# Kernel tuning notes

Hardware: AMD Instinct MI355X
Metric: run time of the kernel (lower is better)

The kernel has to match this reference:

```python
import jax, jax.numpy as jnp
import numpy as np

N = 768        # particles
C0 = 16        # input L0 channels
TDIM = 8       # time embedding channels
NB = 32        # sinusoidal rbf bases
H = 32         # hidden channels per L
NITERS = 2     # diffusion iterations (hk.scan length)
RCUT = 6.0     # rbf length scale
EPS = 1e-8

_lc = np.zeros((3, 3, 3), dtype=np.float32)
_lc[0, 1, 2] = _lc[1, 2, 0] = _lc[2, 0, 1] = 1.0
_lc[0, 2, 1] = _lc[2, 1, 0] = _lc[1, 0, 2] = -1.0
LEVI_CIVITA = jnp.asarray(_lc)


def setup_inputs() -> dict:
    key = jax.random.key(0)
    ks = jax.random.split(key, 20)
    s = 0.05
    inp = {
        "positions":   jax.random.normal(ks[0], (N, 3)),
        "features_L0": jax.random.normal(ks[1], (N, C0, 1)),
        "tw1": s * jax.random.normal(ks[2], (1, 32)),
        "tb1": jnp.zeros((32,)),
        "tw2": s * jax.random.normal(ks[3], (32, TDIM)),
        "tb2": jnp.zeros((TDIM,)),
        "R0_00": s * jax.random.normal(ks[4], (NB, C0 + TDIM)),
        "R0_01": s * jax.random.normal(ks[5], (NB, C0 + TDIM)),
        "W0_L0": s * jax.random.normal(ks[6], (C0 + TDIM, H)),
        "b0_L0": jnp.zeros((H,)),
        "W0_L1": s * jax.random.normal(ks[7], (C0 + TDIM, H)),
        "R1_00":  s * jax.random.normal(ks[8], (NB, H)),
        "R1_11d": s * jax.random.normal(ks[9], (NB, H)),
        "R1_01":  s * jax.random.normal(ks[10], (NB, H)),
        "R1_10":  s * jax.random.normal(ks[11], (NB, H)),
        "R1_11c": s * jax.random.normal(ks[12], (NB, H)),
        "W1_L0": s * jax.random.normal(ks[13], (2 * H, 1)),
        "b1_L0": jnp.zeros((1,)),
        "W1_L1": s * jax.random.normal(ks[14], (3 * H, 2)),
        "hutch_seed": 0,
    }
    return inp


def reference(positions, features_L0, tw1, tb1, tw2, tb2,
              R0_00, R0_01, W0_L0, b0_L0, W0_L1,
              R1_00, R1_11d, R1_01, R1_10, R1_11c,
              W1_L0, b1_L0, W1_L1, hutch_seed):
    freqs = jnp.arange(1, NB + 1, dtype=jnp.float32) * (np.pi / RCUT)
    key0 = jax.random.key(hutch_seed)

    def step(carry, it):
        pos, key = carry
        # pairwise displacements / norms / unit vectors, diagonal masked to 0
        r = pos[:, None, :] - pos[None, :, :]                 # (N,N,3)
        n2 = jnp.sum(r * r, axis=-1)                          # (N,N)
        norms = jnp.sqrt(n2 + EPS)
        valid = n2 > 1e-10
        safe = jnp.where(valid, norms, 1.0)
        unit = r / safe[..., None]                            # (N,N,3)
        # sinusoidal radial basis, masked on diagonal (mask_value = 0)
        rbf = jnp.where(valid[..., None],
                        jnp.sin(norms[..., None] * freqs) / safe[..., None],
                        0.0)                                   # (N,N,NB)
        # time convolution MLP, appended as extra L0 channels
        t = (it.astype(jnp.float32) + 1.0) / NITERS
        th = jax.nn.swish(jnp.array([t]) @ tw1 + tb1)
        tvec = th @ tw2 + tb2                                  # (TDIM,)
        aug = jnp.concatenate(
            [features_L0, jnp.broadcast_to(tvec[None, :, None], (N, TDIM, 1))],
            axis=1)                                            # (N,C0+TDIM,1)
        f0 = aug[..., 0]                                       # (N,C0+TDIM)

        # ---- layer 0: conv (L0 input only) + per-L MLP (nonlinear) ----
        Rw = jnp.einsum('ijb,bc->ijc', rbf, R0_00)
        o0 = jnp.einsum('ijc,jc->ic', Rw, f0)[..., None]       # (N,C,1)
        Rw = jnp.einsum('ijb,bc->ijc', rbf, R0_01)
        o1 = jnp.einsum('ijc,jc,ijm->icm', Rw, f0, unit)       # (N,C,3)
        x0 = jax.nn.swish(jnp.einsum('nco,ch->nho', o0, W0_L0)
                          + b0_L0[None, :, None])              # (N,H,1)
        v1 = jnp.einsum('ncm,ch->nhm', o1, W0_L1)
        gate = jax.nn.sigmoid(jnp.sqrt(jnp.sum(v1 * v1, -1) + EPS))
        x1 = v1 * gate[..., None]                              # (N,H,3)

        # ---- layer 1: full L={0,1} TFN conv + linear output MLPs ----
        f0b = x0[..., 0]
        Rw = jnp.einsum('ijb,bc->ijc', rbf, R1_00)
        o0a = jnp.einsum('ijc,jc->ic', Rw, f0b)                # 0x0->0
        Rw = jnp.einsum('ijb,bc->ijc', rbf, R1_11d)
        o0b = jnp.einsum('ijc,jcm,ijm->ic', Rw, x1, unit)      # 1x1->0 (dot)
        o0 = jnp.concatenate([o0a, o0b], axis=-1)[..., None]   # (N,2H,1)
        Rw = jnp.einsum('ijb,bc->ijc', rbf, R1_01)
        o1a = jnp.einsum('ijc,jc,ijm->icm', Rw, f0b, unit)     # 0x1->1
        Rw = jnp.einsum('ijb,bc->ijc', rbf, R1_10)
        o1b = jnp.einsum('ijc,jcm->icm', Rw, x1)               # 1x0->1
        Rw = jnp.einsum('ijb,bc->ijc', rbf, R1_11c)
        o1c = jnp.einsum('ijc,jca,ijb,abm->icm', Rw, x1, unit, LEVI_CIVITA)  # 1x1->1 (cross)
        o1 = jnp.concatenate([o1a, o1b, o1c], axis=1)          # (N,3H,3)
        y0 = jnp.einsum('nco,ch->nho', o0, W1_L0) + b1_L0[None, :, None]  # (N,1,1)
        y1 = jnp.einsum('ncm,ch->nhm', o1, W1_L1)              # (N,2,3)

        # output head: log-sigma from L0 channel 0, translation from L1 channel 1
        sigmas = jnp.repeat(jnp.exp(y0[:, 0, :]), repeats=3, axis=-1)  # (N,3)
        translations = y1[:, 1, :]
        mu = pos + translations
        key, hkey = jax.random.split(key)
        noise = jax.random.normal(hkey, (N, 3))
        out_y = mu + noise * sigmas
        logp = jax.scipy.stats.norm.logpdf(out_y, loc=mu, scale=sigmas).sum()
        return (out_y, key), (out_y, logp)

    (out_pos, _), (ys, logps) = jax.lax.scan(
        step, (positions, key0), jnp.arange(NITERS))
    out_ys = jnp.concatenate([positions[None], ys], axis=0)   # (NITERS+1,N,3)
    return out_pos, jnp.sum(logps), out_ys
```

## Files before the change

kernel.cpp:

```cpp
#include <hip/hip_runtime.h>
#include <hip/hip_bf16.h>
#include <stdint.h>

#define WS_MODE  0
#define WS_PX    16
#define WS_PY    784
#define WS_PZ    1552
#define WS_TVEC  2320
#define WS_HKEY  2336
#define WS_FEATT 2352
#define WS_W0L0  14640
#define WS_B0L0  15408
#define WS_W0L1  15440
#define WS_W1L0  16208
#define WS_B1L0  16272
#define WS_W1L1  16288
#define WS_R00T  16480
#define WS_R01T  17248
#define WS_R1F   18016
#define WS_GT    23136
#define WS_PA    293472
#define WS_PB    293472
#define WS_LG    735840

#define OUT_LOGP 2304
#define OUT_YS   2305

__device__ __forceinline__ float ld_in(const void* p, int idx, int bf) {
  if (bf) return __bfloat162float(((const __hip_bfloat16*)p)[idx]);
  return ((const float*)p)[idx];
}
__device__ __forceinline__ void store_out(void* out, int idx, float v, int bf) {
  if (bf) ((__hip_bfloat16*)out)[idx] = __float2bfloat16(v);
  else ((float*)out)[idx] = v;
}

__device__ __forceinline__ void tf2x32(uint32_t k0, uint32_t k1, uint32_t x0, uint32_t x1,
                                       uint32_t& o0, uint32_t& o1) {
  uint32_t ks[3] = {k0, k1, k0 ^ k1 ^ 0x1BD11BDAu};
  x0 += ks[0]; x1 += ks[1];
  const int R0[4] = {13, 15, 26, 6};
  const int R1[4] = {17, 29, 16, 24};
#pragma unroll
  for (int i = 0; i < 5; ++i) {
    const int* r = (i & 1) ? R1 : R0;
#pragma unroll
    for (int q = 0; q < 4; ++q) {
      x0 += x1;
      x1 = (x1 << r[q]) | (x1 >> (32 - r[q]));
      x1 ^= x0;
    }
    x0 += ks[(i + 1) % 3];
    x1 += ks[(i + 2) % 3] + (uint32_t)(i + 1);
  }
  o0 = x0; o1 = x1;
}

__device__ __forceinline__ float erfinv_f(float x) {
  float w = -log1pf(-x * x);
  float p;
  if (w < 5.0f) {
    w -= 2.5f;
    p = 2.81022636e-08f;
    p = fmaf(p, w, 3.43273939e-07f);
    p = fmaf(p, w, -3.5233877e-06f);
    p = fmaf(p, w, -4.39150654e-06f);
    p = fmaf(p, w, 0.00021858087f);
    p = fmaf(p, w, -0.00125372503f);
    p = fmaf(p, w, -0.00417768164f);
    p = fmaf(p, w, 0.246640727f);
    p = fmaf(p, w, 1.50140941f);
  } else {
    w = sqrtf(w) - 3.0f;
    p = -0.000200214257f;
    p = fmaf(p, w, 0.000100950558f);
    p = fmaf(p, w, 0.00134934322f);
    p = fmaf(p, w, -0.00367342844f);
    p = fmaf(p, w, 0.00573950773f);
    p = fmaf(p, w, -0.0076224613f);
    p = fmaf(p, w, 0.00943887047f);
    p = fmaf(p, w, 1.00167406f);
    p = fmaf(p, w, 2.83297682f);
  }
  return p * x;
}

__global__ void k_init(const void* pos, const void* feats, const void* tw1, const void* tb1,
                       const void* tw2, const void* tb2, const void* R000, const void* R001,
                       const void* W0L0, const void* b0L0, const void* W0L1,
                       const void* R100, const void* R111d, const void* R101,
                       const void* R110, const void* R111c,
                       const void* W1L0, const void* b1L0, const void* W1L1,
                       const int* seedp, float* ws, void* out) {
  __shared__ int s_ok;
  int tid = threadIdx.x;
  if (tid == 0) s_ok = 1;
  __syncthreads();
  {
    const unsigned short* ph = (const unsigned short*)pos;
    int ok = 1;
    for (int e = tid; e < 2304; e += 256) {
      unsigned short v = ph[e];
      if ((v & 0x7fffu) != 0u) {
        int ex = (v >> 7) & 0xff;
        if (ex < 40 || ex > 140) ok = 0;
      }
    }
    if (!ok) atomicAnd(&s_ok, 0);
  }
  __syncthreads();
  int bf = s_ok;
  if (tid == 0) ws[WS_MODE] = (float)bf;

  for (int n = tid; n < 768; n += 256) {
    ws[WS_PX + n] = ld_in(pos, n * 3 + 0, bf);
    ws[WS_PY + n] = ld_in(pos, n * 3 + 1, bf);
    ws[WS_PZ + n] = ld_in(pos, n * 3 + 2, bf);
  }
  for (int e = tid; e < 2304; e += 256)
    store_out(out, OUT_YS + e, ld_in(pos, e, bf), bf);
  for (int e = tid; e < 12288; e += 256) {
    int j = e >> 4, c = e & 15;
    ws[WS_FEATT + c * 768 + j] = ld_in(feats, e, bf);
  }
  for (int e = tid; e < 768; e += 256) {
    ws[WS_W0L0 + e] = ld_in(W0L0, e, bf);
    ws[WS_W0L1 + e] = ld_in(W0L1, e, bf);
    int b = e / 24, c = e % 24;
    ws[WS_R00T + c * 32 + b] = ld_in(R000, e, bf);
    ws[WS_R01T + c * 32 + b] = ld_in(R001, e, bf);
  }
  for (int e = tid; e < 32; e += 256) ws[WS_B0L0 + e] = ld_in(b0L0, e, bf);
  for (int e = tid; e < 64; e += 256) ws[WS_W1L0 + e] = ld_in(W1L0, e, bf);
  for (int e = tid; e < 192; e += 256) ws[WS_W1L1 + e] = ld_in(W1L1, e, bf);
  if (tid == 0) ws[WS_B1L0] = ld_in(b1L0, 0, bf);
  for (int e = tid; e < 1024; e += 256) {
    ws[WS_R1F + 0 * 1024 + e] = ld_in(R100, e, bf);
    ws[WS_R1F + 1 * 1024 + e] = ld_in(R111d, e, bf);
    ws[WS_R1F + 2 * 1024 + e] = ld_in(R101, e, bf);
    ws[WS_R1F + 3 * 1024 + e] = ld_in(R110, e, bf);
    ws[WS_R1F + 4 * 1024 + e] = ld_in(R111c, e, bf);
  }
  if (tid < 16) {
    int it = tid >> 3, d = tid & 7;
    float t = (float)(it + 1) * 0.5f;
    float a = ld_in(tb2, d, bf);
    for (int h = 0; h < 32; ++h) {
      float pre = fmaf(t, ld_in(tw1, h, bf), ld_in(tb1, h, bf));
      float th = pre / (1.0f + expf(-pre));
      a = fmaf(th, ld_in(tw2, h * 8 + d, bf), a);
    }
    ws[WS_TVEC + it * 8 + d] = a;
  }
  if (tid == 0) {
    uint32_t k0 = 0u, k1 = (uint32_t)seedp[0];
    uint32_t* hk = (uint32_t*)(ws + WS_HKEY);
    uint32_t a0, a1, b0, b1, c0, c1;
    tf2x32(k0, k1, 0u, 0u, a0, a1);
    tf2x32(k0, k1, 0u, 1u, b0, b1);
    hk[0] = b0; hk[1] = b1;
    tf2x32(a0, a1, 0u, 1u, c0, c1);
    hk[2] = c0; hk[3] = c1;
  }
}

template <int CH>
__global__ __launch_bounds__(256) void k_passA(const float* __restrict__ ws,
                                               float* __restrict__ wso, int it) {
  int i = blockIdx.x, jset = blockIdx.y;
  int tid = threadIdx.x, lane = tid & 63, w = tid >> 6;
  int j = jset * 256 + tid;
  float pix = ws[WS_PX + i], piy = ws[WS_PY + i], piz = ws[WS_PZ + i];

  float dx = pix - ws[WS_PX + j];
  float dy = piy - ws[WS_PY + j];
  float dz = piz - ws[WS_PZ + j];
  float n2 = dx * dx + dy * dy + dz * dz;
  float nrm = sqrtf(n2 + 1e-8f);
  float invn = 1.0f / nrm;
  float msk = (n2 > 1e-10f) ? invn : 0.0f;
  float ux = dx * invn, uy = dy * invn, uz = dz * invn;
  float sn, cs;
  sincosf(nrm * 0.52359879f, &sn, &cs);
  float rbf[32];
  float twoc = 2.0f * cs;
  rbf[0] = sn * msk;
  float skm1 = 0.0f, sk = rbf[0];
#pragma unroll
  for (int k = 1; k < 32; ++k) {
    float s2 = fmaf(twoc, sk, -skm1);
    skm1 = sk; sk = s2; rbf[k] = sk;
  }

  float fv[12];
  if (CH == 0) {
#pragma unroll
    for (int c = 0; c < 12; ++c) fv[c] = ws[WS_FEATT + c * 768 + j];
  } else {
#pragma unroll
    for (int c = 0; c < 4; ++c) fv[c] = ws[WS_FEATT + (12 + c) * 768 + j];
#pragma unroll
    for (int c = 4; c < 12; ++c) fv[c] = ws[WS_TVEC + it * 8 + (c - 4)];
  }

  const float* __restrict__ rt0 = ws + WS_R00T + CH * 384;
  const float* __restrict__ rt1 = ws + WS_R01T + CH * 384;
  float out[48];
#pragma unroll
  for (int c = 0; c < 12; ++c) {
    float rw0 = 0.0f, rw1 = 0.0f;
#pragma unroll
    for (int b = 0; b < 32; ++b) {
      rw0 = fmaf(rbf[b], rt0[c * 32 + b], rw0);
      rw1 = fmaf(rbf[b], rt1[c * 32 + b], rw1);
    }
    float f = fv[c];
    out[c] = rw0 * f;
    float pp = rw1 * f;
    out[12 + 3 * c + 0] = pp * ux;
    out[12 + 3 * c + 1] = pp * uy;
    out[12 + 3 * c + 2] = pp * uz;
  }

#pragma unroll
  for (int k = 0; k < 48; ++k) {
    float v = out[k];
    v += __shfl_xor(v, 1);
    v += __shfl_xor(v, 2);
    out[k] = v;
  }
  __shared__ float P[48][65];
  if ((lane & 3) == 0) {
    int col = w * 16 + (lane >> 2);
#pragma unroll
    for (int k = 0; k < 48; ++k) P[k][col] = out[k];
  }
  __syncthreads();
  if (tid < 48) {
    float s = 0.0f;
#pragma unroll 8
    for (int q = 0; q < 64; ++q) s += P[tid][q];
    wso[WS_PA + ((CH * 3 + jset) * 768 + i) * 48 + tid] = s;
  }
}

__global__ __launch_bounds__(64) void k_passA2(const float* __restrict__ ws,
                                               float* __restrict__ wso) {
  int i = blockIdx.x, lane = threadIdx.x;
  __shared__ float oall[96];
  __shared__ float wf[11][32];
#pragma unroll
  for (int rep = 0; rep < 2; ++rep) {
    int t = rep * 64 + lane;
    if (rep == 0 || lane < 32) {
      int ch, k;
      if (t < 24) { ch = t / 12; k = t % 12; }
      else { int u = t - 24; int c = u / 3, m = u % 3; ch = c / 12; k = 12 + 3 * (c % 12) + m; }
      float s = 0.0f;
#pragma unroll
      for (int js = 0; js < 3; ++js)
        s += ws[WS_PA + ((ch * 3 + js) * 768 + i) * 48 + k];
      oall[t] = s;
    }
  }
  __syncthreads();
  if (lane < 32) {
    int h = lane;
    float x0p = ws[WS_B0L0 + h];
#pragma unroll
    for (int c = 0; c < 24; ++c) x0p = fmaf(oall[c], ws[WS_W0L0 + c * 32 + h], x0p);
    float f0b = x0p / (1.0f + expf(-x0p));
    float v0 = 0.0f, v1 = 0.0f, v2 = 0.0f;
#pragma unroll
    for (int c = 0; c < 24; ++c) {
      float w = ws[WS_W0L1 + c * 32 + h];
      v0 = fmaf(oall[24 + 3 * c + 0], w, v0);
      v1 = fmaf(oall[24 + 3 * c + 1], w, v1);
      v2 = fmaf(oall[24 + 3 * c + 2], w, v2);
    }
    float g = 1.0f / (1.0f + expf(-sqrtf(v0 * v0 + v1 * v1 + v2 * v2 + 1e-8f)));
    float x1m0 = v0 * g, x1m1 = v1 * g, x1m2 = v2 * g;
    float WA = ws[WS_W1L0 + h];
    float WB = ws[WS_W1L0 + 32 + h];
    float Wa = ws[WS_W1L1 + h * 2 + 1];
    float Wb = ws[WS_W1L1 + (32 + h) * 2 + 1];
    float Wc = ws[WS_W1L1 + (64 + h) * 2 + 1];
    wf[0][h] = WA * f0b;
    wf[1][h] = WB * x1m0; wf[2][h] = WB * x1m1; wf[3][h] = WB * x1m2;
    wf[4][h] = Wa * f0b;
    wf[5][h] = Wb * x1m0; wf[6][h] = Wb * x1m1; wf[7][h] = Wb * x1m2;
    wf[8][h] = Wc * x1m0; wf[9][h] = Wc * x1m1; wf[10][h] = Wc * x1m2;
  }
  __syncthreads();
  for (int tt = lane; tt < 352; tt += 64) {
    int comp = tt >> 5, b = tt & 31;
    int tab = (comp == 0) ? 0 : (comp < 4) ? 1 : (comp == 4) ? 2 : (comp < 8) ? 3 : 4;
    const float* rrow = ws + WS_R1F + tab * 1024 + b * 32;
    float gacc = 0.0f;
#pragma unroll
    for (int c = 0; c < 32; ++c) gacc = fmaf(rrow[c], wf[comp][c], gacc);
    wso[WS_GT + i * 352 + tt] = gacc;
  }
}

__global__ __launch_bounds__(256) void k_passB(const float* __restrict__ ws,
                                               float* __restrict__ wso) {
  int i = blockIdx.y * 256 + threadIdx.x;
  int chunk = blockIdx.x;
  float pix = ws[WS_PX + i], piy = ws[WS_PY + i], piz = ws[WS_PZ + i];
  float y0 = 0.0f, t0 = 0.0f, t1 = 0.0f, t2 = 0.0f;
  for (int q = 0; q < 8; ++q) {
    int j = chunk * 8 + q;
    float dx = pix - ws[WS_PX + j];
    float dy = piy - ws[WS_PY + j];
    float dz = piz - ws[WS_PZ + j];
    float n2 = dx * dx + dy * dy + dz * dz;
    float nrm = sqrtf(n2 + 1e-8f);
    float invn = 1.0f / nrm;
    float msk = (n2 > 1e-10f) ? invn : 0.0f;
    float ux = dx * invn, uy = dy * invn, uz = dz * invn;
    float sn, cs;
    sincosf(nrm * 0.52359879f, &sn, &cs);
    float rbf[32];
    float twoc = 2.0f * cs;
    rbf[0] = sn * msk;
    float skm1 = 0.0f, sk = rbf[0];
#pragma unroll
    for (int k = 1; k < 32; ++k) {
      float s2 = fmaf(twoc, sk, -skm1);
      skm1 = sk; sk = s2; rbf[k] = sk;
    }
    const float* g = ws + WS_GT + j * 352;
    float sA = 0.f, vB0 = 0.f, vB1 = 0.f, vB2 = 0.f, sC = 0.f;
    float vD0 = 0.f, vD1 = 0.f, vD2 = 0.f, vE0 = 0.f, vE1 = 0.f, vE2 = 0.f;
#pragma unroll
    for (int b = 0; b < 32; ++b) {
      float r = rbf[b];
      sA  = fmaf(r, g[0 * 32 + b], sA);
      vB0 = fmaf(r, g[1 * 32 + b], vB0);
      vB1 = fmaf(r, g[2 * 32 + b], vB1);
      vB2 = fmaf(r, g[3 * 32 + b], vB2);
      sC  = fmaf(r, g[4 * 32 + b], sC);
      vD0 = fmaf(r, g[5 * 32 + b], vD0);
      vD1 = fmaf(r, g[6 * 32 + b], vD1);
      vD2 = fmaf(r, g[7 * 32 + b], vD2);
      vE0 = fmaf(r, g[8 * 32 + b], vE0);
      vE1 = fmaf(r, g[9 * 32 + b], vE1);
      vE2 = fmaf(r, g[10 * 32 + b], vE2);
    }
    y0 += sA + vB0 * ux + vB1 * uy + vB2 * uz;
    t0 += sC * ux + vD0 + (vE1 * uz - vE2 * uy);
    t1 += sC * uy + vD1 + (vE2 * ux - vE0 * uz);
    t2 += sC * uz + vD2 + (vE0 * uy - vE1 * ux);
  }
  float4* pb = (float4*)(wso + WS_PB);
  pb[i * 96 + chunk] = make_float4(y0, t0, t1, t2);
}

__global__ __launch_bounds__(64) void k_passB2(float* __restrict__ ws, void* out, int it) {
  int i = blockIdx.x * 64 + threadIdx.x;
  int bf = (int)ws[WS_MODE];
  const float4* pb = (const float4*)(ws + WS_PB);
  float ax = 0.f, ay = 0.f, az = 0.f, aw = 0.f;
#pragma unroll 8
  for (int c = 0; c < 96; ++c) {
    float4 v = pb[i * 96 + c];
    ax += v.x; ay += v.y; az += v.z; aw += v.w;
  }
  float y0 = ax + ws[WS_B1L0];
  float sg = expf(y0);
  float s2 = sg * sg;
  float lnrm = 0.5f * logf(6.2831855f * s2);
  const uint32_t* hk = (const uint32_t*)(ws + WS_HKEY);
  uint32_t h0 = hk[it * 2 + 0], h1 = hk[it * 2 + 1];
  float base[3] = {ws[WS_PX + i], ws[WS_PY + i], ws[WS_PZ + i]};
  float tr[3] = {ay, az, aw};
  float logp = 0.0f;
#pragma unroll
  for (int m = 0; m < 3; ++m) {
    float mu = base[m] + tr[m];
    int f = i * 3 + m;
    uint32_t o0, o1;
    tf2x32(h0, h1, 0u, (uint32_t)f, o0, o1);
    uint32_t bits = o0 ^ o1;
    float u1 = __uint_as_float((bits >> 9) | 0x3f800000u) - 1.0f;
    const float lo = -0.99999994f;
    float u = fmaxf(lo, u1 * 2.0f + lo);
    float nz = 1.41421354f * erfinv_f(u);
    float oy = mu + nz * sg;
    float d = oy - mu;
    logp -= lnrm + (d * d) / (2.0f * s2);
    if (m == 0) ws[WS_PX + i] = oy;
    else if (m == 1) ws[WS_PY + i] = oy;
    else ws[WS_PZ + i] = oy;
    store_out(out, OUT_YS + (it + 1) * 2304 + i * 3 + m, oy, bf);
    if (it == 1) store_out(out, i * 3 + m, oy, bf);
  }
  ws[WS_LG + it * 768 + i] = logp;
}

__global__ void k_logp(float* __restrict__ ws, void* out) {
  __shared__ float red[256];
  int t = threadIdx.x;
  float s = 0.0f;
  for (int e = t; e < 1536; e += 256) s += ws[WS_LG + e];
  red[t] = s;
  __syncthreads();
  for (int off = 128; off; off >>= 1) {
    if (t < off) red[t] += red[t + off];
    __syncthreads();
  }
  if (t == 0) store_out(out, OUT_LOGP, red[0], (int)ws[WS_MODE]);
}

extern "C" void kernel_launch(void* const* d_in, const int* in_sizes, int n_in,
                              void* d_out, int out_size, void* d_ws, size_t ws_size,
                              hipStream_t stream) {
  (void)in_sizes; (void)n_in; (void)out_size; (void)ws_size;
  float* ws = (float*)d_ws;
  k_init<<<1, 256, 0, stream>>>(d_in[0], d_in[1], d_in[2], d_in[3], d_in[4], d_in[5],
                                d_in[6], d_in[7], d_in[8], d_in[9], d_in[10],
                                d_in[11], d_in[12], d_in[13], d_in[14], d_in[15],
                                d_in[16], d_in[17], d_in[18], (const int*)d_in[19],
                                ws, d_out);
  for (int it = 0; it < 2; ++it) {
    k_passA<0><<<dim3(768, 3), 256, 0, stream>>>(ws, ws, it);
    k_passA<1><<<dim3(768, 3), 256, 0, stream>>>(ws, ws, it);
    k_passA2<<<768, 64, 0, stream>>>(ws, ws);
    k_passB<<<dim3(96, 3), 256, 0, stream>>>(ws, ws);
    k_passB2<<<12, 64, 0, stream>>>(ws, d_out, it);
  }
  k_logp<<<1, 256, 0, stream>>>(ws, d_out);
}
```

Measured before the change: 223.5 us.

## Parallelize init across blocks and merge passA channels with in-thread j-loop

```diff
diff --git a/kernel.cpp b/kernel.cpp
--- a/kernel.cpp
+++ b/kernel.cpp
@@ -85,141 +85,178 @@
   return p * x;
 }
 
-__global__ void k_init(const void* pos, const void* feats, const void* tw1, const void* tb1,
-                       const void* tw2, const void* tb2, const void* R000, const void* R001,
-                       const void* W0L0, const void* b0L0, const void* W0L1,
-                       const void* R100, const void* R111d, const void* R101,
-                       const void* R110, const void* R111c,
-                       const void* W1L0, const void* b1L0, const void* W1L1,
-                       const int* seedp, float* ws, void* out) {
+__device__ int probe_bf(const void* pos, int tid) {
   __shared__ int s_ok;
-  int tid = threadIdx.x;
   if (tid == 0) s_ok = 1;
   __syncthreads();
-  {
-    const unsigned short* ph = (const unsigned short*)pos;
-    int ok = 1;
-    for (int e = tid; e < 2304; e += 256) {
-      unsigned short v = ph[e];
-      if ((v & 0x7fffu) != 0u) {
-        int ex = (v >> 7) & 0xff;
-        if (ex < 40 || ex > 140) ok = 0;
-      }
-    }
-    if (!ok) atomicAnd(&s_ok, 0);
-  }
-  __syncthreads();
-  int bf = s_ok;
-  if (tid == 0) ws[WS_MODE] = (float)bf;
-
-  for (int n = tid; n < 768; n += 256) {
-    ws[WS_PX + n] = ld_in(pos, n * 3 + 0, bf);
-    ws[WS_PY + n] = ld_in(pos, n * 3 + 1, bf);
-    ws[WS_PZ + n] = ld_in(pos, n * 3 + 2, bf);
-  }
-  for (int e = tid; e < 2304; e += 256)
-    store_out(out, OUT_YS + e, ld_in(pos, e, bf), bf);
-  for (int e = tid; e < 12288; e += 256) {
-    int j = e >> 4, c = e & 15;
-    ws[WS_FEATT + c * 768 + j] = ld_in(feats, e, bf);
-  }
-  for (int e = tid; e < 768; e += 256) {
-    ws[WS_W0L0 + e] = ld_in(W0L0, e, bf);
-    ws[WS_W0L1 + e] = ld_in(W0L1, e, bf);
-    int b = e / 24, c = e % 24;
-    ws[WS_R00T + c * 32 + b] = ld_in(R000, e, bf);
-    ws[WS_R01T + c * 32 + b] = ld_in(R001, e, bf);
-  }
-  for (int e = tid; e < 32; e += 256) ws[WS_B0L0 + e] = ld_in(b0L0, e, bf);
-  for (int e = tid; e < 64; e += 256) ws[WS_W1L0 + e] = ld_in(W1L0, e, bf);
-  for (int e = tid; e < 192; e += 256) ws[WS_W1L1 + e] = ld_in(W1L1, e, bf);
-  if (tid == 0) ws[WS_B1L0] = ld_in(b1L0, 0, bf);
-  for (int e = tid; e < 1024; e += 256) {
-    ws[WS_R1F + 0 * 1024 + e] = ld_in(R100, e, bf);
-    ws[WS_R1F + 1 * 1024 + e] = ld_in(R111d, e, bf);
-    ws[WS_R1F + 2 * 1024 + e] = ld_in(R101, e, bf);
-    ws[WS_R1F + 3 * 1024 + e] = ld_in(R110, e, bf);
-    ws[WS_R1F + 4 * 1024 + e] = ld_in(R111c, e, bf);
-  }
-  if (tid < 16) {
-    int it = tid >> 3, d = tid & 7;
-    float t = (float)(it + 1) * 0.5f;
-    float a = ld_in(tb2, d, bf);
-    for (int h = 0; h < 32; ++h) {
-      float pre = fmaf(t, ld_in(tw1, h, bf), ld_in(tb1, h, bf));
-      float th = pre / (1.0f + expf(-pre));
-      a = fmaf(th, ld_in(tw2, h * 8 + d, bf), a);
-    }
-    ws[WS_TVEC + it * 8 + d] = a;
-  }
-  if (tid == 0) {
-    uint32_t k0 = 0u, k1 = (uint32_t)seedp[0];
-    uint32_t* hk = (uint32_t*)(ws + WS_HKEY);
-    uint32_t a0, a1, b0, b1, c0, c1;
-    tf2x32(k0, k1, 0u, 0u, a0, a1);
-    tf2x32(k0, k1, 0u, 1u, b0, b1);
-    hk[0] = b0; hk[1] = b1;
-    tf2x32(a0, a1, 0u, 1u, c0, c1);
-    hk[2] = c0; hk[3] = c1;
-  }
-}
-
-template <int CH>
+  const unsigned short* ph = (const unsigned short*)pos;
+  int ok = 1;
+  for (int e = tid; e < 2304; e += 256) {
+    unsigned short v = ph[e];
+    if ((v & 0x7fffu) != 0u) {
+      int ex = (v >> 7) & 0xff;
+      if (ex < 40 || ex > 140) ok = 0;
+    }
+  }
+  if (!ok) atomicAnd(&s_ok, 0);
+  __syncthreads();
+  return s_ok;
+}
+
+__global__ __launch_bounds__(256) void k_init(
+    const void* pos, const void* feats, const void* tw1, const void* tb1,
+    const void* tw2, const void* tb2, const void* R000, const void* R001,
+    const void* W0L0, const void* b0L0, const void* W0L1,
+    const void* R100, const void* R111d, const void* R101,
+    const void* R110, const void* R111c,
+    const void* W1L0, const void* b1L0, const void* W1L1,
+    const int* seedp, float* ws, void* out) {
+  int tid = threadIdx.x, b = blockIdx.x;
+  int bf = probe_bf(pos, tid);
+  switch (b) {
+    case 0: {
+      if (tid == 0) ws[WS_MODE] = (float)bf;
+      if (tid < 16) {
+        int it = tid >> 3, d = tid & 7;
+        float t = (float)(it + 1) * 0.5f;
+        float a = ld_in(tb2, d, bf);
+        for (int h = 0; h < 32; ++h) {
+          float pre = fmaf(t, ld_in(tw1, h, bf), ld_in(tb1, h, bf));
+          float th = pre / (1.0f + expf(-pre));
+          a = fmaf(th, ld_in(tw2, h * 8 + d, bf), a);
+        }
+        ws[WS_TVEC + it * 8 + d] = a;
+      }
+      if (tid == 32) {
+        uint32_t k0 = 0u, k1 = (uint32_t)seedp[0];
+        uint32_t* hk = (uint32_t*)(ws + WS_HKEY);
+        uint32_t a0, a1, b0, b1, c0, c1;
+        tf2x32(k0, k1, 0u, 0u, a0, a1);
+        tf2x32(k0, k1, 0u, 1u, b0, b1);
+        hk[0] = b0; hk[1] = b1;
+        tf2x32(a0, a1, 0u, 1u, c0, c1);
+        hk[2] = c0; hk[3] = c1;
+      }
+      break;
+    }
+    case 1: {
+      for (int n = tid; n < 768; n += 256) {
+        ws[WS_PX + n] = ld_in(pos, n * 3 + 0, bf);
+        ws[WS_PY + n] = ld_in(pos, n * 3 + 1, bf);
+        ws[WS_PZ + n] = ld_in(pos, n * 3 + 2, bf);
+      }
+      break;
+    }
+    case 2: case 3: {
+      for (int e = (b - 2) * 1152 + tid; e < (b - 1) * 1152; e += 256)
+        store_out(out, OUT_YS + e, ld_in(pos, e, bf), bf);
+      break;
+    }
+    case 4: case 5: case 6: case 7:
+    case 8: case 9: case 10: case 11: {
+      int base = (b - 4) * 1536;
+      for (int e = base + tid; e < base + 1536; e += 256) {
+        int j = e >> 4, c = e & 15;
+        ws[WS_FEATT + c * 768 + j] = ld_in(feats, e, bf);
+      }
+      break;
+    }
+    case 12: {
+      for (int e = tid; e < 768; e += 256) {
+        ws[WS_W0L0 + e] = ld_in(W0L0, e, bf);
+        ws[WS_W0L1 + e] = ld_in(W0L1, e, bf);
+        int bb = e / 24, c = e % 24;
+        ws[WS_R00T + c * 32 + bb] = ld_in(R000, e, bf);
+        ws[WS_R01T + c * 32 + bb] = ld_in(R001, e, bf);
+      }
+      break;
+    }
+    case 13: {
+      if (tid < 32) ws[WS_B0L0 + tid] = ld_in(b0L0, tid, bf);
+      if (tid >= 64 && tid < 128) ws[WS_W1L0 + tid - 64] = ld_in(W1L0, tid - 64, bf);
+      if (tid >= 128 && tid < 192) {
+        for (int e = tid - 128; e < 192; e += 64) ws[WS_W1L1 + e] = ld_in(W1L1, e, bf);
+      }
+      if (tid == 33) ws[WS_B1L0] = ld_in(b1L0, 0, bf);
+      break;
+    }
+    case 14: case 15: {
+      int base = (b - 14) * 2560;
+      const void* tabs[5] = {R100, R111d, R101, R110, R111c};
+      for (int e = base + tid; e < base + 2560; e += 256) {
+        int tab = e >> 10, off = e & 1023;
+        ws[WS_R1F + e] = ld_in(tabs[tab], off, bf);
+      }
+      break;
+    }
+  }
+}
+
 __global__ __launch_bounds__(256) void k_passA(const float* __restrict__ ws,
                                                float* __restrict__ wso, int it) {
-  int i = blockIdx.x, jset = blockIdx.y;
+  int i = blockIdx.x, CH = blockIdx.y;
   int tid = threadIdx.x, lane = tid & 63, w = tid >> 6;
-  int j = jset * 256 + tid;
   float pix = ws[WS_PX + i], piy = ws[WS_PY + i], piz = ws[WS_PZ + i];
-
-  float dx = pix - ws[WS_PX + j];
-  float dy = piy - ws[WS_PY + j];
-  float dz = piz - ws[WS_PZ + j];
-  float n2 = dx * dx + dy * dy + dz * dz;
-  float nrm = sqrtf(n2 + 1e-8f);
-  float invn = 1.0f / nrm;
-  float msk = (n2 > 1e-10f) ? invn : 0.0f;
-  float ux = dx * invn, uy = dy * invn, uz = dz * invn;
-  float sn, cs;
-  sincosf(nrm * 0.52359879f, &sn, &cs);
-  float rbf[32];
-  float twoc = 2.0f * cs;
-  rbf[0] = sn * msk;
-  float skm1 = 0.0f, sk = rbf[0];
-#pragma unroll
-  for (int k = 1; k < 32; ++k) {
-    float s2 = fmaf(twoc, sk, -skm1);
-    skm1 = sk; sk = s2; rbf[k] = sk;
-  }
-
-  float fv[12];
-  if (CH == 0) {
-#pragma unroll
-    for (int c = 0; c < 12; ++c) fv[c] = ws[WS_FEATT + c * 768 + j];
-  } else {
-#pragma unroll
-    for (int c = 0; c < 4; ++c) fv[c] = ws[WS_FEATT + (12 + c) * 768 + j];
-#pragma unroll
-    for (int c = 4; c < 12; ++c) fv[c] = ws[WS_TVEC + it * 8 + (c - 4)];
-  }
 
   const float* __restrict__ rt0 = ws + WS_R00T + CH * 384;
   const float* __restrict__ rt1 = ws + WS_R01T + CH * 384;
+
+  float tvv[8];
+#pragma unroll
+  for (int d = 0; d < 8; ++d) tvv[d] = ws[WS_TVEC + it * 8 + d];
+
   float out[48];
 #pragma unroll
-  for (int c = 0; c < 12; ++c) {
-    float rw0 = 0.0f, rw1 = 0.0f;
-#pragma unroll
-    for (int b = 0; b < 32; ++b) {
-      rw0 = fmaf(rbf[b], rt0[c * 32 + b], rw0);
-      rw1 = fmaf(rbf[b], rt1[c * 32 + b], rw1);
-    }
-    float f = fv[c];
-    out[c] = rw0 * f;
-    float pp = rw1 * f;
-    out[12 + 3 * c + 0] = pp * ux;
-    out[12 + 3 * c + 1] = pp * uy;
-    out[12 + 3 * c + 2] = pp * uz;
+  for (int k = 0; k < 48; ++k) out[k] = 0.0f;
+
+  for (int jset = 0; jset < 3; ++jset) {
+    int j = jset * 256 + tid;
+    float dx = pix - ws[WS_PX + j];
+    float dy = piy - ws[WS_PY + j];
+    float dz = piz - ws[WS_PZ + j];
+    float n2 = dx * dx + dy * dy + dz * dz;
+    float nrm = sqrtf(n2 + 1e-8f);
+    float invn = 1.0f / nrm;
+    float msk = (n2 > 1e-10f) ? invn : 0.0f;
+    float ux = dx * invn, uy = dy * invn, uz = dz * invn;
+    float sn, cs;
+    sincosf(nrm * 0.52359879f, &sn, &cs);
+    float rbf[32];
+    float twoc = 2.0f * cs;
+    rbf[0] = sn * msk;
+    float skm1 = 0.0f, sk = rbf[0];
+#pragma unroll
+    for (int k = 1; k < 32; ++k) {
+      float s2 = fmaf(twoc, sk, -skm1);
+      skm1 = sk; sk = s2; rbf[k] = sk;
+    }
+
+    float fv[12];
+    if (CH == 0) {
+#pragma unroll
+      for (int c = 0; c < 12; ++c) fv[c] = ws[WS_FEATT + c * 768 + j];
+    } else {
+#pragma unroll
+      for (int c = 0; c < 4; ++c) fv[c] = ws[WS_FEATT + (12 + c) * 768 + j];
+#pragma unroll
+      for (int c = 4; c < 12; ++c) fv[c] = tvv[c - 4];
+    }
+
+#pragma unroll
+    for (int c = 0; c < 12; ++c) {
+      float rw0 = 0.0f, rw1 = 0.0f;
+#pragma unroll
+      for (int bq = 0; bq < 32; ++bq) {
+        rw0 = fmaf(rbf[bq], rt0[c * 32 + bq], rw0);
+        rw1 = fmaf(rbf[bq], rt1[c * 32 + bq], rw1);
+      }
+      float f = fv[c];
+      out[c] = fmaf(rw0, f, out[c]);
+      float pp = rw1 * f;
+      out[12 + 3 * c + 0] = fmaf(pp, ux, out[12 + 3 * c + 0]);
+      out[12 + 3 * c + 1] = fmaf(pp, uy, out[12 + 3 * c + 1]);
+      out[12 + 3 * c + 2] = fmaf(pp, uz, out[12 + 3 * c + 2]);
+    }
   }
 
 #pragma unroll
@@ -240,7 +277,7 @@
     float s = 0.0f;
 #pragma unroll 8
     for (int q = 0; q < 64; ++q) s += P[tid][q];
-    wso[WS_PA + ((CH * 3 + jset) * 768 + i) * 48 + tid] = s;
+    wso[WS_PA + (CH * 768 + i) * 48 + tid] = s;
   }
 }
 
@@ -256,11 +293,7 @@
       int ch, k;
       if (t < 24) { ch = t / 12; k = t % 12; }
       else { int u = t - 24; int c = u / 3, m = u % 3; ch = c / 12; k = 12 + 3 * (c % 12) + m; }
-      float s = 0.0f;
-#pragma unroll
-      for (int js = 0; js < 3; ++js)
-        s += ws[WS_PA + ((ch * 3 + js) * 768 + i) * 48 + k];
-      oall[t] = s;
+      oall[t] = ws[WS_PA + (ch * 768 + i) * 48 + k];
     }
   }
   __syncthreads();
@@ -418,14 +451,13 @@
                               hipStream_t stream) {
   (void)in_sizes; (void)n_in; (void)out_size; (void)ws_size;
   float* ws = (float*)d_ws;
-  k_init<<<1, 256, 0, stream>>>(d_in[0], d_in[1], d_in[2], d_in[3], d_in[4], d_in[5],
-                                d_in[6], d_in[7], d_in[8], d_in[9], d_in[10],
-                                d_in[11], d_in[12], d_in[13], d_in[14], d_in[15],
-                                d_in[16], d_in[17], d_in[18], (const int*)d_in[19],
-                                ws, d_out);
+  k_init<<<16, 256, 0, stream>>>(d_in[0], d_in[1], d_in[2], d_in[3], d_in[4], d_in[5],
+                                 d_in[6], d_in[7], d_in[8], d_in[9], d_in[10],
+                                 d_in[11], d_in[12], d_in[13], d_in[14], d_in[15],
+                                 d_in[16], d_in[17], d_in[18], (const int*)d_in[19],
+                                 ws, d_out);
   for (int it = 0; it < 2; ++it) {
-    k_passA<0><<<dim3(768, 3), 256, 0, stream>>>(ws, ws, it);
-    k_passA<1><<<dim3(768, 3), 256, 0, stream>>>(ws, ws, it);
+    k_passA<<<dim3(768, 2), 256, 0, stream>>>(ws, ws, it);
     k_passA2<<<768, 64, 0, stream>>>(ws, ws);
     k_passB<<<dim3(96, 3), 256, 0, stream>>>(ws, ws);
     k_passB2<<<12, 64, 0, stream>>>(ws, d_out, it);
```

After: 266.6 us. 1.19x slower.
